# Kernel optimization log

Hardware: AMD Instinct MI355X
Metric: run time of the kernel (lower is better)

Reference implementation:

```python
import jax, jax.numpy as jnp
import numpy as np

D_MODEL = 2048
NHEADS = 16
ROPE_DIM = 64      # config.rope['head_dim']
NOPE_DIM = 128     # config.nope_head_dim
V_DIM = 128        # config.v_head_dim
Q_LORA = 1536      # config.q_lora_rank
KV_LORA = 512      # config.kv_lora_rank
ROPE_BASE = 10000.0
EPS = 1e-6
Q_HEAD = NOPE_DIM + ROPE_DIM   # 192
KV_HEAD = NOPE_DIM + V_DIM     # 256


def rms_norm(x, w):
    return x * jax.lax.rsqrt(jnp.mean(x * x, axis=-1, keepdims=True) + EPS) * w


def apply_rope(x, offset=0):
    # x: (B, H, T, d); standard rotate-half RoPE, positions offset by past length
    d, t = x.shape[-1], x.shape[2]
    inv_freq = 1.0 / (ROPE_BASE ** (jnp.arange(0, d, 2, dtype=jnp.float32) / d))
    pos = jnp.arange(offset, offset + t, dtype=jnp.float32)
    f = pos[:, None] * inv_freq[None, :]          # (T, d/2)
    cos = jnp.concatenate([jnp.cos(f), jnp.cos(f)], -1).astype(x.dtype)
    sin = jnp.concatenate([jnp.sin(f), jnp.sin(f)], -1).astype(x.dtype)
    x1, x2 = jnp.split(x, 2, axis=-1)
    rot = jnp.concatenate([-x2, x1], -1)
    return x * cos + rot * sin


def setup_inputs() -> dict:
    key = jax.random.key(0)
    ks = jax.random.split(key, 8)
    s = 0.02
    return {
        'x': jax.random.normal(ks[0], (2, 2048, D_MODEL), jnp.float32),
        'q_a_w': jax.random.normal(ks[1], (D_MODEL, Q_LORA), jnp.float32) * s,
        'q_a_norm_w': jnp.ones((Q_LORA,), jnp.float32),
        'q_b_w': jax.random.normal(ks[2], (Q_LORA, NHEADS * Q_HEAD), jnp.float32) * s,
        'kv_a_w': jax.random.normal(ks[3], (D_MODEL, KV_LORA + ROPE_DIM), jnp.float32) * s,
        'kv_norm_w': jnp.ones((KV_LORA,), jnp.float32),
        'kv_b_w': jax.random.normal(ks[4], (KV_LORA, NHEADS * KV_HEAD), jnp.float32) * s,
        'o_w': jax.random.normal(ks[5], (NHEADS * V_DIM, D_MODEL), jnp.float32) * s,
    }


def reference(x, q_a_w, q_a_norm_w, q_b_w, kv_a_w, kv_norm_w, kv_b_w, o_w):
    B, T, _ = x.shape
    # Query: LoRA down-proj -> RMSNorm -> up-proj
    q = rms_norm(x @ q_a_w, q_a_norm_w) @ q_b_w            # (B,T,H*Q_HEAD)
    q = q.reshape(B, T, NHEADS, Q_HEAD).transpose(0, 2, 1, 3)
    q_nope, q_rope = q[..., :NOPE_DIM], q[..., NOPE_DIM:]
    # KV: joint compressed projection, split into latent + shared rope key
    kv = x @ kv_a_w                                         # (B,T,KV_LORA+ROPE_DIM)
    kv_c, k_rope = kv[..., :KV_LORA], kv[..., KV_LORA:]
    k_rope = k_rope[:, None, :, :]                          # (B,1,T,ROPE_DIM) - MQA rope key
    kvb = rms_norm(kv_c, kv_norm_w) @ kv_b_w                # (B,T,H*KV_HEAD)
    kvb = kvb.reshape(B, T, NHEADS, KV_HEAD).transpose(0, 2, 1, 3)
    k_nope, v = kvb[..., :NOPE_DIM], kvb[..., NOPE_DIM:]
    # Decoupled RoPE (prefill: offset 0)
    q_rope = apply_rope(q_rope)
    k_rope = apply_rope(k_rope)
    qs = jnp.concatenate([q_nope, q_rope], -1)              # (B,H,T,Q_HEAD)
    ks = jnp.concatenate([k_nope, jnp.broadcast_to(k_rope, (B, NHEADS, T, ROPE_DIM))], -1)
    # SDPA with causal mask, scale = 1/sqrt(q_head_dim)
    scale = 1.0 / np.sqrt(Q_HEAD).astype(np.float32)
    scores = jnp.einsum('bhqd,bhkd->bhqk', qs, ks) * scale
    mask = jnp.tril(jnp.ones((T, T), bool))
    scores = jnp.where(mask[None, None], scores, jnp.finfo(scores.dtype).min)
    attn = jax.nn.softmax(scores, axis=-1)
    out = jnp.einsum('bhqk,bhkd->bhqd', attn, v)            # (B,H,T,V_DIM)
    out = out.transpose(0, 2, 1, 3).reshape(B, T, NHEADS * V_DIM)
    return out @ o_w                                        # (B,T,d_model)
```

## Files before the change

### kernel.cpp

```cpp
#include <hip/hip_runtime.h>
#include <hip/hip_bf16.h>
#include <math.h>

#define NHEADS 16
#define SEQ 2048
#define BATCH 2
#define NTOK (BATCH * SEQ)
#define EPSF 1e-6f

typedef short bf16x8 __attribute__((ext_vector_type(8)));
typedef float f32x4 __attribute__((ext_vector_type(4)));

__device__ __forceinline__ unsigned short f2bf(float v) {
    __hip_bfloat16 h = __float2bfloat16(v);
    return *reinterpret_cast<unsigned short*>(&h);
}
__device__ __forceinline__ float bf2f(unsigned short u) {
    __hip_bfloat16 h = *reinterpret_cast<__hip_bfloat16*>(&u);
    return __bfloat162float(h);
}
__device__ __forceinline__ void g2l16(const void* g, void* l) {
    __builtin_amdgcn_global_load_lds(
        (const __attribute__((address_space(1))) void*)g,
        (__attribute__((address_space(3))) void*)l, 16, 0, 0);
}

#define ROPE_L2 0.4152410118609203f

struct WSeg { const float* src; unsigned short* dst; int Nw, K, nx, off; };
struct WSegs { WSeg s[5]; };
#define CVT_OFF 15104

__global__ __launch_bounds__(256) void prep_weights(
    WSegs segs, const float* __restrict__ x, unsigned short* __restrict__ x_bf)
{
    const int bid = blockIdx.x;
    const int tid = threadIdx.x;
    if (bid >= CVT_OFF) {
        const int i = (bid - CVT_OFF) * 256 + tid;
        float4 a = ((const float4*)x)[i * 2];
        float4 b = ((const float4*)x)[i * 2 + 1];
        unsigned short o[8] = {f2bf(a.x), f2bf(a.y), f2bf(a.z), f2bf(a.w),
                               f2bf(b.x), f2bf(b.y), f2bf(b.z), f2bf(b.w)};
        *(bf16x8*)(x_bf + (size_t)i * 8) = *(bf16x8*)o;
        return;
    }
    __shared__ float T[32][33];
    int si = 0;
#pragma unroll
    for (int i = 1; i < 5; ++i) si += (bid >= segs.s[i].off) ? 1 : 0;
    const WSeg sg = segs.s[si];
    const int local = bid - sg.off;
    const int bx = local % sg.nx, by = local / sg.nx;
    const int n0 = bx * 32, k0 = by * 32;
    const int r = tid >> 3, c4 = (tid & 7) * 4;
    const bool valid = (n0 < sg.Nw);
    if (valid) {
        float4 v = *(const float4*)(sg.src + (size_t)(k0 + r) * sg.Nw + n0 + c4);
        T[r][c4 + 0] = v.x; T[r][c4 + 1] = v.y; T[r][c4 + 2] = v.z; T[r][c4 + 3] = v.w;
    }
    __syncthreads();
    unsigned short o[4];
#pragma unroll
    for (int j = 0; j < 4; ++j) o[j] = valid ? f2bf(T[c4 + j][r]) : (unsigned short)0;
    *(ulong1*)(sg.dst + (size_t)(n0 + r) * sg.K + k0 + c4) = *(ulong1*)o;
}

#define GSTAGE(AS, BS, BUF, T)                                                  \
    do {                                                                        \
        const int k0_ = (T) * 32;                                               \
        _Pragma("unroll")                                                       \
        for (int t_ = 0; t_ < 2; ++t_) {                                        \
            const int chunk_ = t_ * 256 + tid;                                  \
            const int row_ = chunk_ >> 2, koff_ = (chunk_ & 3) << 3;            \
            g2l16(A  + (size_t)(bm + row_) * K + k0_ + koff_, (char*)AS[BUF] + chunk_ * 16); \
            g2l16(Bt + (size_t)(bn + row_) * K + k0_ + koff_, (char*)BS[BUF] + chunk_ * 16); \
        }                                                                       \
    } while (0)

template <int OUT_BF16>
__global__ __launch_bounds__(256) void gemm_bt(
    const unsigned short* __restrict__ A,
    const unsigned short* __restrict__ Bt,
    void* __restrict__ Cv,
    int K, int N)
{
    __shared__ __align__(16) unsigned short As[2][128 * 32];
    __shared__ __align__(16) unsigned short Bs[2][128 * 32];
    const int tid = threadIdx.x;
    const int lane = tid & 63, wid = tid >> 6;
    const int l16 = lane & 15, lq = lane >> 4;
    const int wr = wid >> 1, wc = wid & 1;
    const int bm = blockIdx.y * 128, bn = blockIdx.x * 128;

    f32x4 acc[4][4];
#pragma unroll
    for (int m = 0; m < 4; ++m)
#pragma unroll
        for (int n = 0; n < 4; ++n) acc[m][n] = (f32x4){0.f, 0.f, 0.f, 0.f};

    const int nk = K >> 5;
    GSTAGE(As, Bs, 0, 0);
    int cur = 0;
    for (int t = 0; t < nk; ++t) {
        __syncthreads();
        if (t + 1 < nk) GSTAGE(As, Bs, cur ^ 1, t + 1);

        bf16x8 af[4], bfr[4];
#pragma unroll
        for (int m = 0; m < 4; ++m)
            af[m] = *(const bf16x8*)(As[cur] + (wr * 64 + m * 16 + l16) * 32 + lq * 8);
#pragma unroll
        for (int n = 0; n < 4; ++n)
            bfr[n] = *(const bf16x8*)(Bs[cur] + (wc * 64 + n * 16 + l16) * 32 + lq * 8);
#pragma unroll
        for (int m = 0; m < 4; ++m)
#pragma unroll
            for (int n = 0; n < 4; ++n)
                acc[m][n] = __builtin_amdgcn_mfma_f32_16x16x32_bf16(af[m], bfr[n], acc[m][n], 0, 0, 0);
        cur ^= 1;
    }

#pragma unroll
    for (int m = 0; m < 4; ++m)
#pragma unroll
        for (int n = 0; n < 4; ++n)
#pragma unroll
            for (int reg = 0; reg < 4; ++reg) {
                const int row = bm + wr * 64 + m * 16 + lq * 4 + reg;
                const int col = bn + wc * 64 + n * 16 + l16;
                if (OUT_BF16) ((unsigned short*)Cv)[(size_t)row * N + col] = f2bf(acc[m][n][reg]);
                else          ((float*)Cv)[(size_t)row * N + col] = acc[m][n][reg];
            }
}

__global__ __launch_bounds__(256) void gemm_stage2(
    const unsigned short* __restrict__ qa,
    const unsigned short* __restrict__ wqb,
    unsigned short* __restrict__ qbuf,
    const unsigned short* __restrict__ kvc,
    const unsigned short* __restrict__ wkvb,
    unsigned short* __restrict__ kvb,
    unsigned short* __restrict__ vt)
{
    __shared__ __align__(16) unsigned short As[2][128 * 32];
    __shared__ __align__(16) unsigned short Bs[2][128 * 32];
    const int bid = blockIdx.x;
    const int tid = threadIdx.x;
    const int lane = tid & 63, wid = tid >> 6;
    const int l16 = lane & 15, lq = lane >> 4;
    const int wr = wid >> 1, wc = wid & 1;

    const bool is_q = bid < 768;
    const unsigned short* A;
    const unsigned short* Bt;
    int K, N, bm, bn;
    if (is_q) { A = qa;  Bt = wqb;  K = 1536; N = 3072; bn = (bid % 24) * 128;        bm = (bid / 24) * 128; }
    else      { A = kvc; Bt = wkvb; K = 512;  N = 4096; bn = ((bid - 768) % 32) * 128; bm = ((bid - 768) / 32) * 128; }

    f32x4 acc[4][4];
#pragma unroll
    for (int m = 0; m < 4; ++m)
#pragma unroll
        for (int n = 0; n < 4; ++n) acc[m][n] = (f32x4){0.f, 0.f, 0.f, 0.f};

    const int nk = K >> 5;
    GSTAGE(As, Bs, 0, 0);
    int cur = 0;
    for (int t = 0; t < nk; ++t) {
        __syncthreads();
        if (t + 1 < nk) GSTAGE(As, Bs, cur ^ 1, t + 1);

        bf16x8 af[4], bfr[4];
#pragma unroll
        for (int m = 0; m < 4; ++m)
            af[m] = *(const bf16x8*)(As[cur] + (wr * 64 + m * 16 + l16) * 32 + lq * 8);
#pragma unroll
        for (int n = 0; n < 4; ++n)
            bfr[n] = *(const bf16x8*)(Bs[cur] + (wc * 64 + n * 16 + l16) * 32 + lq * 8);
#pragma unroll
        for (int m = 0; m < 4; ++m)
#pragma unroll
            for (int n = 0; n < 4; ++n)
                acc[m][n] = __builtin_amdgcn_mfma_f32_16x16x32_bf16(af[m], bfr[n], acc[m][n], 0, 0, 0);
        cur ^= 1;
    }

    const bool is_v = (!is_q) && ((bn & 255) == 128);
    if (!is_v) {
        unsigned short* C = is_q ? qbuf : kvb;
#pragma unroll
        for (int m = 0; m < 4; ++m)
#pragma unroll
            for (int n = 0; n < 4; ++n)
#pragma unroll
                for (int reg = 0; reg < 4; ++reg) {
                    const int row = bm + wr * 64 + m * 16 + lq * 4 + reg;
                    const int col = bn + wc * 64 + n * 16 + l16;
                    C[(size_t)row * N + col] = f2bf(acc[m][n][reg]);
                }
    } else {
        const int h = bn >> 8;
#pragma unroll
        for (int m = 0; m < 4; ++m)
#pragma unroll
            for (int n = 0; n < 4; ++n) {
                const int d = wc * 64 + n * 16 + l16;
                const int tok0 = bm + wr * 64 + m * 16 + lq * 4;
                const int b_ = tok0 >> 11, s_ = tok0 & (SEQ - 1);
                unsigned short pk[4];
#pragma unroll
                for (int reg = 0; reg < 4; ++reg) pk[reg] = f2bf(acc[m][n][reg]);
                *(ulong1*)(vt + (((size_t)(b_ * NHEADS + h) * 128 + d) * SEQ + s_)) = *(ulong1*)pk;
            }
    }
}

__global__ __launch_bounds__(256) void norms_fused(
    const float* __restrict__ qkv, const float* __restrict__ qw,
    const float* __restrict__ kvw,
    unsigned short* __restrict__ qa_out, unsigned short* __restrict__ kv_out,
    unsigned short* __restrict__ krope_out)
{
    const int bid = blockIdx.x;
    const int tid = threadIdx.x;
    __shared__ float wsum[4];
    __shared__ float s_scale;
    const int wave = tid >> 6;

    if (bid < 4096) {
        const int row = bid;
        const float* p = qkv + (size_t)row * 2176;
        float ss = 0.f;
#pragma unroll
        for (int t = 0; t < 6; ++t) { float v = p[tid + t * 256]; ss += v * v; }
#pragma unroll
        for (int off = 32; off > 0; off >>= 1) ss += __shfl_down(ss, off, 64);
        if ((tid & 63) == 0) wsum[wave] = ss;
        __syncthreads();
        if (tid == 0) {
            float t = wsum[0] + wsum[1] + wsum[2] + wsum[3];
            s_scale = rsqrtf(t / 1536.0f + EPSF);
        }
        __syncthreads();
        const float sc = s_scale;
#pragma unroll
        for (int t = 0; t < 6; ++t) {
            int c = tid + t * 256;
            qa_out[(size_t)row * 1536 + c] = f2bf(p[c] * sc * qw[c]);
        }
    } else {
        const int row = bid - 4096;
        const float* p = qkv + (size_t)row * 2176 + 1536;
        float v0 = p[tid], v1 = p[tid + 256];
        float ss = v0 * v0 + v1 * v1;
#pragma unroll
        for (int off = 32; off > 0; off >>= 1) ss += __shfl_down(ss, off, 64);
        if ((tid & 63) == 0) wsum[wave] = ss;
        __syncthreads();
        if (tid == 0) {
            float t = wsum[0] + wsum[1] + wsum[2] + wsum[3];
            s_scale = rsqrtf(t / 512.0f + EPSF);
        }
        __syncthreads();
        const float sc = s_scale;
        kv_out[(size_t)row * 512 + tid]       = f2bf(v0 * sc * kvw[tid]);
        kv_out[(size_t)row * 512 + tid + 256] = f2bf(v1 * sc * kvw[tid + 256]);
        if (tid < 64) {
            const int s = row & (SEQ - 1);
            const int j = tid, jj = j & 31;
            float inv = exp2f(-ROPE_L2 * (float)jj);
            float f = (float)s * inv;
            float sn, cs;
            sincosf(f, &sn, &cs);
            const float* kb = p + 512;
            float v = (j < 32) ? (kb[j] * cs - kb[j + 32] * sn)
                               : (kb[j] * cs + kb[j - 32] * sn);
            krope_out[(size_t)row * 64 + j] = f2bf(v);
        }
    }
}

#define KPD 200
#define VPD 76
#define PPD 76
#define RESCALE_THR 8.0f

__global__ __launch_bounds__(256) void flash_mfma(
    const unsigned short* __restrict__ qbuf,
    const unsigned short* __restrict__ kvb,
    const unsigned short* __restrict__ krope,
    const unsigned short* __restrict__ vt,
    unsigned short* __restrict__ ctx)
{
    __shared__ __align__(16) unsigned short Ks[64][KPD];
    __shared__ __align__(16) unsigned short Vs[144][VPD];
    __shared__ __align__(16) unsigned short Ps[4][16][PPD];
    const int id = blockIdx.x;
    const int xcd = id & 7, sl = id >> 3;
    const int grp = sl >> 4, pair = sl & 15;
    const int hb = xcd + 8 * grp;
    const int h = hb & 15, b = hb >> 4;
    const int tid = threadIdx.x;
    const int wid = tid >> 6, lane = tid & 63;
    const int l16 = lane & 15, lq = lane >> 4;

    const size_t headV = (size_t)(b * NHEADS + h) * 128 * SEQ;
    const float scale = 0.07216878364870323f;

    float cs8[8], sn8[8];
    const int vrow = tid >> 1, vg = tid & 1;

    {
        int r = 128 + (tid >> 4);
        int c = (tid & 15) * 4;
        unsigned short v = (tid >> 4) == 0 ? (unsigned short)0x3F80 : (unsigned short)0;
        Vs[r][c] = v; Vs[r][c + 1] = v; Vs[r][c + 2] = v; Vs[r][c + 3] = v;
    }

#pragma unroll
    for (int pass = 0; pass < 2; ++pass) {
        const int qt = pass ? (31 - pair) : pair;
        const int srow = qt * 64 + wid * 16 + l16;

        bf16x8 qf[6];
        {
            const unsigned short* qp = qbuf + (size_t)(b * SEQ + srow) * 3072 + h * 192 + lq * 8;
            bf16x8 raw[6];
#pragma unroll
            for (int kk = 0; kk < 6; ++kk) raw[kk] = *(const bf16x8*)(qp + kk * 32);
#pragma unroll
            for (int jj = 0; jj < 8; ++jj) {
                float inv = exp2f(-ROPE_L2 * (float)(lq * 8 + jj));
                float fp = (float)srow * inv;
                sn8[jj] = __sinf(fp);
                cs8[jj] = __cosf(fp);
            }
#pragma unroll
            for (int kk = 0; kk < 4; ++kk) {
                unsigned short o[8];
#pragma unroll
                for (int e = 0; e < 8; ++e) o[e] = f2bf(bf2f(((unsigned short*)&raw[kk])[e]) * scale);
                qf[kk] = *(bf16x8*)o;
            }
            unsigned short o4[8], o5[8];
#pragma unroll
            for (int e = 0; e < 8; ++e) {
                float x1 = bf2f(((unsigned short*)&raw[4])[e]);
                float x2 = bf2f(((unsigned short*)&raw[5])[e]);
                o4[e] = f2bf((x1 * cs8[e] - x2 * sn8[e]) * scale);
                o5[e] = f2bf((x2 * cs8[e] + x1 * sn8[e]) * scale);
            }
            qf[4] = *(bf16x8*)o4;
            qf[5] = *(bf16x8*)o5;
        }

        f32x4 o[8];
#pragma unroll
        for (int f = 0; f < 8; ++f) o[f] = (f32x4){0.f, 0.f, 0.f, 0.f};
        f32x4 oS = (f32x4){0.f, 0.f, 0.f, 0.f};
        float m[4] = {-1e30f, -1e30f, -1e30f, -1e30f};

        const int nkt = qt + 1;
        for (int kt = 0; kt < nkt; ++kt) {
            __syncthreads();
            {
                const int tk0 = b * SEQ + kt * 64;
#pragma unroll
                for (int t = 0; t < 4; ++t) {
                    int i = tid + t * 256;
                    int r = i >> 4, c8 = i & 15;
                    *(bf16x8*)&Ks[r][c8 * 8] =
                        *(const bf16x8*)(kvb + (size_t)(tk0 + r) * 4096 + h * 256 + c8 * 8);
                }
#pragma unroll
                for (int t = 0; t < 2; ++t) {
                    int i = tid + t * 256;
                    int r = i >> 3, c8 = i & 7;
                    *(bf16x8*)&Ks[r][128 + c8 * 8] =
                        *(const bf16x8*)(krope + (size_t)(tk0 + r) * 64 + c8 * 8);
                }
                const unsigned short* vsrc = vt + headV + (size_t)vrow * SEQ + kt * 64 + vg * 8;
#pragma unroll
                for (int j = 0; j < 4; ++j)
                    *(bf16x8*)&Vs[vrow][(vg + j * 2) * 8] = *(const bf16x8*)(vsrc + j * 16);
            }
            __syncthreads();

            f32x4 s[4];
#pragma unroll
            for (int f = 0; f < 4; ++f) s[f] = (f32x4){0.f, 0.f, 0.f, 0.f};
            __builtin_amdgcn_s_setprio(1);
#pragma unroll
            for (int f = 0; f < 4; ++f) {
#pragma unroll
                for (int kk = 0; kk < 6; ++kk) {
                    bf16x8 bfr = *(const bf16x8*)&Ks[f * 16 + l16][kk * 32 + lq * 8];
                    s[f] = __builtin_amdgcn_mfma_f32_16x16x32_bf16(qf[kk], bfr, s[f], 0, 0, 0);
                }
            }
            __builtin_amdgcn_s_setprio(0);

            const int qabs = qt * 64 + wid * 16 + lq * 4;
            const bool diag = (kt == qt);
            float rmax4[4];
#pragma unroll
            for (int reg = 0; reg < 4; ++reg) {
                if (diag) {
                    int q = qabs + reg;
                    int k0 = kt * 64 + l16;
                    if (k0      > q) s[0][reg] = -1e30f;
                    if (k0 + 16 > q) s[1][reg] = -1e30f;
                    if (k0 + 32 > q) s[2][reg] = -1e30f;
                    if (k0 + 48 > q) s[3][reg] = -1e30f;
                }
                float rmax = fmaxf(fmaxf(s[0][reg], s[1][reg]), fmaxf(s[2][reg], s[3][reg]));
                rmax = fmaxf(rmax, __shfl_xor(rmax, 1, 64));
                rmax = fmaxf(rmax, __shfl_xor(rmax, 2, 64));
                rmax = fmaxf(rmax, __shfl_xor(rmax, 4, 64));
                rmax = fmaxf(rmax, __shfl_xor(rmax, 8, 64));
                rmax4[reg] = rmax;
            }
            float dmx = fmaxf(fmaxf(rmax4[0] - m[0], rmax4[1] - m[1]),
                              fmaxf(rmax4[2] - m[2], rmax4[3] - m[3]));
            if (!__all(dmx <= RESCALE_THR)) {
#pragma unroll
                for (int reg = 0; reg < 4; ++reg) {
                    float mnew = fmaxf(m[reg], rmax4[reg]);
                    float al = __expf(m[reg] - mnew);
                    m[reg] = mnew;
#pragma unroll
                    for (int f = 0; f < 8; ++f) o[f][reg] *= al;
                    oS[reg] *= al;
                }
            }
#pragma unroll
            for (int reg = 0; reg < 4; ++reg) {
                Ps[wid][lq * 4 + reg][ 0 + l16] = f2bf(__expf(s[0][reg] - m[reg]));
                Ps[wid][lq * 4 + reg][16 + l16] = f2bf(__expf(s[1][reg] - m[reg]));
                Ps[wid][lq * 4 + reg][32 + l16] = f2bf(__expf(s[2][reg] - m[reg]));
                Ps[wid][lq * 4 + reg][48 + l16] = f2bf(__expf(s[3][reg] - m[reg]));
            }

            bf16x8 pa0 = *(const bf16x8*)&Ps[wid][l16][lq * 8];
            bf16x8 pa1 = *(const bf16x8*)&Ps[wid][l16][32 + lq * 8];
            __builtin_amdgcn_s_setprio(1);
#pragma unroll
            for (int f = 0; f < 8; ++f) {
                bf16x8 b0 = *(const bf16x8*)&Vs[f * 16 + l16][lq * 8];
                bf16x8 b1 = *(const bf16x8*)&Vs[f * 16 + l16][32 + lq * 8];
                o[f] = __builtin_amdgcn_mfma_f32_16x16x32_bf16(pa0, b0, o[f], 0, 0, 0);
                o[f] = __builtin_amdgcn_mfma_f32_16x16x32_bf16(pa1, b1, o[f], 0, 0, 0);
            }
            {
                bf16x8 s0 = *(const bf16x8*)&Vs[128 + l16][lq * 8];
                bf16x8 s1 = *(const bf16x8*)&Vs[128 + l16][32 + lq * 8];
                oS = __builtin_amdgcn_mfma_f32_16x16x32_bf16(pa0, s0, oS, 0, 0, 0);
                oS = __builtin_amdgcn_mfma_f32_16x16x32_bf16(pa1, s1, oS, 0, 0, 0);
            }
            __builtin_amdgcn_s_setprio(0);
        }

#pragma unroll
        for (int reg = 0; reg < 4; ++reg) {
            float ls = __shfl(oS[reg], lane & 48, 64);
            float inv = 1.0f / ls;
            unsigned short* dst = ctx + (size_t)(b * SEQ + qt * 64 + wid * 16 + lq * 4 + reg) * 2048 + h * 128 + l16;
#pragma unroll
            for (int f = 0; f < 8; ++f) dst[f * 16] = f2bf(o[f][reg] * inv);
        }
    }
}

extern "C" void kernel_launch(void* const* d_in, const int* in_sizes, int n_in,
                              void* d_out, int out_size, void* d_ws, size_t ws_size,
                              hipStream_t stream) {
    const float* x          = (const float*)d_in[0];
    const float* q_a_w      = (const float*)d_in[1];
    const float* q_a_norm_w = (const float*)d_in[2];
    const float* q_b_w      = (const float*)d_in[3];
    const float* kv_a_w     = (const float*)d_in[4];
    const float* kv_norm_w  = (const float*)d_in[5];
    const float* kv_b_w     = (const float*)d_in[6];
    const float* o_w        = (const float*)d_in[7];
    float* out = (float*)d_out;

    char* ws = (char*)d_ws;
    float*          qkv_cat  = (float*)(ws + 0);
    unsigned short* ctx_bf   = (unsigned short*)(ws + 0);
    unsigned short* qbuf_bf  = (unsigned short*)(ws + 35651584);
    unsigned short* vt_bf    = (unsigned short*)(ws + 60817408);
    unsigned short* kvb_bf   = (unsigned short*)(ws + 77594624);
    unsigned short* x_bf     = (unsigned short*)(ws + 111149056);
    unsigned short* q_a_bf   = (unsigned short*)(ws + 111149056);
    unsigned short* kv_c_bf  = (unsigned short*)(ws + 127926272);
    unsigned short* krope_bf = (unsigned short*)(ws + 132120576);
    unsigned short* wcat     = (unsigned short*)(ws + 132644864);
    unsigned short* wkva_t   = wcat + (size_t)1536 * 2048;
    unsigned short* wqb_t    = (unsigned short*)(ws + 141557760);
    unsigned short* wkvb_t   = (unsigned short*)(ws + 150994944);
    unsigned short* wo_t     = (unsigned short*)(ws + 155189248);

    dim3 blk(256);

    WSegs segs;
    segs.s[0] = { q_a_w,  wcat,   1536, 2048,  48,     0 };
    segs.s[1] = { q_b_w,  wqb_t,  3072, 1536,  96,  3072 };
    segs.s[2] = { kv_a_w, wkva_t,  576, 2048,  20,  7680 };
    segs.s[3] = { kv_b_w, wkvb_t, 4096,  512, 128,  8960 };
    segs.s[4] = { o_w,    wo_t,   2048, 2048,  64, 11008 };
    prep_weights<<<CVT_OFF + 4096, blk, 0, stream>>>(segs, x, x_bf);

    gemm_bt<0><<<dim3(17, 32), blk, 0, stream>>>(x_bf, wcat, qkv_cat, 2048, 2176);

    norms_fused<<<8192, blk, 0, stream>>>(qkv_cat, q_a_norm_w, kv_norm_w,
                                          q_a_bf, kv_c_bf, krope_bf);

    gemm_stage2<<<1792, blk, 0, stream>>>(q_a_bf, wqb_t, qbuf_bf,
                                          kv_c_bf, wkvb_t, kvb_bf, vt_bf);

    flash_mfma<<<dim3(512), blk, 0, stream>>>(qbuf_bf, kvb_bf, krope_bf, vt_bf, ctx_bf);

    gemm_bt<0><<<dim3(16, 32), blk, 0, stream>>>(ctx_bf, wo_t, out, 2048, 2048);
}
```

Baseline: 329.8 us.

## Compute transposed S tile to keep P in registers, drop LDS round-trip

Swaps the MFMA operand order so each lane holds scores for one query row across keys, letting softmax probabilities be packed straight into the PV MFMA A-operand registers with v_cvt_pk_bf16 instead of going through a shared-memory P buffer. The row sum is now accumulated in registers rather than by an extra ones-column MFMA, and V is loaded with a permuted key order to match the new register layout. The aim is to remove LDS writes and reads, barriers and the extra MFMAs per tile. The cost is more complex V loads (8-byte gathers) and extra shuffles when rescaling.

```diff
diff --git a/kernel.cpp b/kernel.cpp
--- a/kernel.cpp
+++ b/kernel.cpp
@@ -23,6 +23,11 @@
     __builtin_amdgcn_global_load_lds(
         (const __attribute__((address_space(1))) void*)g,
         (__attribute__((address_space(3))) void*)l, 16, 0, 0);
+}
+__device__ __forceinline__ unsigned cvt_pk_bf16(float lo, float hi) {
+    unsigned r;
+    asm volatile("v_cvt_pk_bf16_f32 %0, %1, %2" : "=v"(r) : "v"(lo), "v"(hi));
+    return r;
 }
 
 #define ROPE_L2 0.4152410118609203f
@@ -283,7 +288,6 @@
 
 #define KPD 200
 #define VPD 76
-#define PPD 76
 #define RESCALE_THR 8.0f
 
 __global__ __launch_bounds__(256) void flash_mfma(
@@ -294,8 +298,7 @@
     unsigned short* __restrict__ ctx)
 {
     __shared__ __align__(16) unsigned short Ks[64][KPD];
-    __shared__ __align__(16) unsigned short Vs[144][VPD];
-    __shared__ __align__(16) unsigned short Ps[4][16][PPD];
+    __shared__ __align__(16) unsigned short Vs[128][VPD];
     const int id = blockIdx.x;
     const int xcd = id & 7, sl = id >> 3;
     const int grp = sl >> 4, pair = sl & 15;
@@ -311,13 +314,6 @@
     float cs8[8], sn8[8];
     const int vrow = tid >> 1, vg = tid & 1;
 
-    {
-        int r = 128 + (tid >> 4);
-        int c = (tid & 15) * 4;
-        unsigned short v = (tid >> 4) == 0 ? (unsigned short)0x3F80 : (unsigned short)0;
-        Vs[r][c] = v; Vs[r][c + 1] = v; Vs[r][c + 2] = v; Vs[r][c + 3] = v;
-    }
-
 #pragma unroll
     for (int pass = 0; pass < 2; ++pass) {
         const int qt = pass ? (31 - pair) : pair;
@@ -358,8 +354,8 @@
         f32x4 o[8];
 #pragma unroll
         for (int f = 0; f < 8; ++f) o[f] = (f32x4){0.f, 0.f, 0.f, 0.f};
-        f32x4 oS = (f32x4){0.f, 0.f, 0.f, 0.f};
-        float m[4] = {-1e30f, -1e30f, -1e30f, -1e30f};
+        float m = -1e30f;
+        float lsum = 0.f;
 
         const int nkt = qt + 1;
         for (int kt = 0; kt < nkt; ++kt) {
@@ -380,10 +376,16 @@
                     *(bf16x8*)&Ks[r][128 + c8 * 8] =
                         *(const bf16x8*)(krope + (size_t)(tk0 + r) * 64 + c8 * 8);
                 }
-                const unsigned short* vsrc = vt + headV + (size_t)vrow * SEQ + kt * 64 + vg * 8;
-#pragma unroll
-                for (int j = 0; j < 4; ++j)
-                    *(bf16x8*)&Vs[vrow][(vg + j * 2) * 8] = *(const bf16x8*)(vsrc + j * 16);
+                const unsigned short* vbase = vt + headV + (size_t)vrow * SEQ + kt * 64;
+#pragma unroll
+                for (int j = 0; j < 4; ++j) {
+                    int g = vg + 2 * j;
+                    int kA = (g & 3) * 4 + (g >> 2) * 32;
+                    unsigned long long pk[2];
+                    pk[0] = *(const unsigned long long*)(vbase + kA);
+                    pk[1] = *(const unsigned long long*)(vbase + kA + 16);
+                    *(bf16x8*)&Vs[vrow][g * 8] = *(const bf16x8*)pk;
+                }
             }
             __syncthreads();
 
@@ -395,55 +397,68 @@
             for (int f = 0; f < 4; ++f) {
 #pragma unroll
                 for (int kk = 0; kk < 6; ++kk) {
-                    bf16x8 bfr = *(const bf16x8*)&Ks[f * 16 + l16][kk * 32 + lq * 8];
-                    s[f] = __builtin_amdgcn_mfma_f32_16x16x32_bf16(qf[kk], bfr, s[f], 0, 0, 0);
+                    bf16x8 kfr = *(const bf16x8*)&Ks[f * 16 + l16][kk * 32 + lq * 8];
+                    s[f] = __builtin_amdgcn_mfma_f32_16x16x32_bf16(kfr, qf[kk], s[f], 0, 0, 0);
                 }
             }
             __builtin_amdgcn_s_setprio(0);
 
-            const int qabs = qt * 64 + wid * 16 + lq * 4;
-            const bool diag = (kt == qt);
-            float rmax4[4];
-#pragma unroll
-            for (int reg = 0; reg < 4; ++reg) {
-                if (diag) {
-                    int q = qabs + reg;
-                    int k0 = kt * 64 + l16;
-                    if (k0      > q) s[0][reg] = -1e30f;
-                    if (k0 + 16 > q) s[1][reg] = -1e30f;
-                    if (k0 + 32 > q) s[2][reg] = -1e30f;
-                    if (k0 + 48 > q) s[3][reg] = -1e30f;
+            if (kt == qt) {
+                const int kb0 = kt * 64 + lq * 4;
+#pragma unroll
+                for (int f = 0; f < 4; ++f)
+#pragma unroll
+                    for (int reg = 0; reg < 4; ++reg)
+                        if (kb0 + f * 16 + reg > srow) s[f][reg] = -1e30f;
+            }
+
+            float rmax = fmaxf(fmaxf(s[0][0], s[0][1]), fmaxf(s[0][2], s[0][3]));
+            rmax = fmaxf(rmax, fmaxf(fmaxf(s[1][0], s[1][1]), fmaxf(s[1][2], s[1][3])));
+            rmax = fmaxf(rmax, fmaxf(fmaxf(s[2][0], s[2][1]), fmaxf(s[2][2], s[2][3])));
+            rmax = fmaxf(rmax, fmaxf(fmaxf(s[3][0], s[3][1]), fmaxf(s[3][2], s[3][3])));
+            rmax = fmaxf(rmax, __shfl_xor(rmax, 16, 64));
+            rmax = fmaxf(rmax, __shfl_xor(rmax, 32, 64));
+
+            if (!__all(rmax - m <= RESCALE_THR)) {
+                float mnew = fmaxf(m, rmax);
+                float al = __expf(m - mnew);
+                m = mnew;
+                lsum *= al;
+#pragma unroll
+                for (int reg = 0; reg < 4; ++reg) {
+                    float ar = __shfl(al, (lane & 48) | (lq * 4 + reg), 64);
+#pragma unroll
+                    for (int f = 0; f < 8; ++f) o[f][reg] *= ar;
                 }
-                float rmax = fmaxf(fmaxf(s[0][reg], s[1][reg]), fmaxf(s[2][reg], s[3][reg]));
-                rmax = fmaxf(rmax, __shfl_xor(rmax, 1, 64));
-                rmax = fmaxf(rmax, __shfl_xor(rmax, 2, 64));
-                rmax = fmaxf(rmax, __shfl_xor(rmax, 4, 64));
-                rmax = fmaxf(rmax, __shfl_xor(rmax, 8, 64));
-                rmax4[reg] = rmax;
-            }
-            float dmx = fmaxf(fmaxf(rmax4[0] - m[0], rmax4[1] - m[1]),
-                              fmaxf(rmax4[2] - m[2], rmax4[3] - m[3]));
-            if (!__all(dmx <= RESCALE_THR)) {
-#pragma unroll
-                for (int reg = 0; reg < 4; ++reg) {
-                    float mnew = fmaxf(m[reg], rmax4[reg]);
-                    float al = __expf(m[reg] - mnew);
-                    m[reg] = mnew;
-#pragma unroll
-                    for (int f = 0; f < 8; ++f) o[f][reg] *= al;
-                    oS[reg] *= al;
-                }
-            }
-#pragma unroll
-            for (int reg = 0; reg < 4; ++reg) {
-                Ps[wid][lq * 4 + reg][ 0 + l16] = f2bf(__expf(s[0][reg] - m[reg]));
-                Ps[wid][lq * 4 + reg][16 + l16] = f2bf(__expf(s[1][reg] - m[reg]));
-                Ps[wid][lq * 4 + reg][32 + l16] = f2bf(__expf(s[2][reg] - m[reg]));
-                Ps[wid][lq * 4 + reg][48 + l16] = f2bf(__expf(s[3][reg] - m[reg]));
-            }
-
-            bf16x8 pa0 = *(const bf16x8*)&Ps[wid][l16][lq * 8];
-            bf16x8 pa1 = *(const bf16x8*)&Ps[wid][l16][32 + lq * 8];
+            }
+
+            unsigned d0[2], d1[2], d2[2], d3[2];
+            float psum = 0.f;
+            {
+                float p0, p1, p2, p3;
+                p0 = __expf(s[0][0] - m); p1 = __expf(s[0][1] - m);
+                p2 = __expf(s[0][2] - m); p3 = __expf(s[0][3] - m);
+                psum += (p0 + p1) + (p2 + p3);
+                d0[0] = cvt_pk_bf16(p0, p1); d0[1] = cvt_pk_bf16(p2, p3);
+                p0 = __expf(s[1][0] - m); p1 = __expf(s[1][1] - m);
+                p2 = __expf(s[1][2] - m); p3 = __expf(s[1][3] - m);
+                psum += (p0 + p1) + (p2 + p3);
+                d1[0] = cvt_pk_bf16(p0, p1); d1[1] = cvt_pk_bf16(p2, p3);
+                p0 = __expf(s[2][0] - m); p1 = __expf(s[2][1] - m);
+                p2 = __expf(s[2][2] - m); p3 = __expf(s[2][3] - m);
+                psum += (p0 + p1) + (p2 + p3);
+                d2[0] = cvt_pk_bf16(p0, p1); d2[1] = cvt_pk_bf16(p2, p3);
+                p0 = __expf(s[3][0] - m); p1 = __expf(s[3][1] - m);
+                p2 = __expf(s[3][2] - m); p3 = __expf(s[3][3] - m);
+                psum += (p0 + p1) + (p2 + p3);
+                d3[0] = cvt_pk_bf16(p0, p1); d3[1] = cvt_pk_bf16(p2, p3);
+            }
+            lsum += psum;
+            unsigned pk0[4] = {d0[0], d0[1], d1[0], d1[1]};
+            unsigned pk1[4] = {d2[0], d2[1], d3[0], d3[1]};
+            bf16x8 pa0 = *(const bf16x8*)pk0;
+            bf16x8 pa1 = *(const bf16x8*)pk1;
+
             __builtin_amdgcn_s_setprio(1);
 #pragma unroll
             for (int f = 0; f < 8; ++f) {
@@ -452,18 +467,15 @@
                 o[f] = __builtin_amdgcn_mfma_f32_16x16x32_bf16(pa0, b0, o[f], 0, 0, 0);
                 o[f] = __builtin_amdgcn_mfma_f32_16x16x32_bf16(pa1, b1, o[f], 0, 0, 0);
             }
-            {
-                bf16x8 s0 = *(const bf16x8*)&Vs[128 + l16][lq * 8];
-                bf16x8 s1 = *(const bf16x8*)&Vs[128 + l16][32 + lq * 8];
-                oS = __builtin_amdgcn_mfma_f32_16x16x32_bf16(pa0, s0, oS, 0, 0, 0);
-                oS = __builtin_amdgcn_mfma_f32_16x16x32_bf16(pa1, s1, oS, 0, 0, 0);
-            }
             __builtin_amdgcn_s_setprio(0);
         }
 
+        float Lf = lsum;
+        Lf += __shfl_xor(Lf, 16, 64);
+        Lf += __shfl_xor(Lf, 32, 64);
 #pragma unroll
         for (int reg = 0; reg < 4; ++reg) {
-            float ls = __shfl(oS[reg], lane & 48, 64);
+            float ls = __shfl(Lf, (lane & 48) | (lq * 4 + reg), 64);
             float inv = 1.0f / ls;
             unsigned short* dst = ctx + (size_t)(b * SEQ + qt * 64 + wid * 16 + lq * 4 + reg) * 2048 + h * 128 + l16;
 #pragma unroll
```

Result: no change. 328.7 us (-0.3%).
